# Performance work log

Hardware: AMD Instinct MI355X
Metric: run time of the kernel (lower is better)

The kernel has to match this reference:

```python
import jax, jax.numpy as jnp
import numpy as np

NUM_GRAPHS = 512


def setup_inputs() -> dict:
    key = jax.random.key(0)
    ks = jax.random.split(key, 16)
    N, E = 50000, 800000
    x = jax.random.normal(ks[0], (N, 3), dtype=jnp.float32)
    edge_index = jax.random.randint(ks[1], (2, E), 0, N, dtype=jnp.int64)
    batch = jnp.sort(jax.random.randint(ks[2], (N,), 0, NUM_GRAPHS, dtype=jnp.int64))

    def glorot(k, shape):
        fan_in, fan_out = shape
        lim = (6.0 / (fan_in + fan_out)) ** 0.5
        return jax.random.uniform(k, shape, jnp.float32, -lim, lim)

    return {
        "x": x, "edge_index": edge_index, "batch": batch,
        "W1": glorot(ks[3], (3, 32)),   "b1": jnp.zeros((32,), jnp.float32),
        "W2": glorot(ks[4], (32, 64)),  "b2": jnp.zeros((64,), jnp.float32),
        "W3": glorot(ks[5], (64, 128)), "b3": jnp.zeros((128,), jnp.float32),
        "Wf1": glorot(ks[6], (128, 32)), "bf1": jnp.zeros((32,), jnp.float32),
        "Wf2": glorot(ks[7], (32, 4)),   "bf2": jnp.zeros((4,), jnp.float32),
    }


def _gcn_conv(x, src, dst, norm, W, b, N):
    # GCNConv: h = x W, then symmetric-normalized aggregation, then bias.
    h = x @ W                                   # [N, out]
    msg = h[src] * norm[:, None]                # [E+N, out] gathered edge messages
    out = jax.ops.segment_sum(msg, dst, num_segments=N)
    return out + b


def reference(x, edge_index, batch, W1, b1, W2, b2, W3, b3, Wf1, bf1, Wf2, bf2):
    N = x.shape[0]
    loops = jnp.arange(N, dtype=edge_index.dtype)
    src = jnp.concatenate([edge_index[0], loops])   # add self-loops (GCNConv default)
    dst = jnp.concatenate([edge_index[1], loops])
    # symmetric normalization deg^-1/2[src] * deg^-1/2[dst], deg counted on dst
    deg = jax.ops.segment_sum(jnp.ones_like(dst, dtype=x.dtype), dst, num_segments=N)
    dinv = jnp.where(deg > 0, jax.lax.rsqrt(deg), 0.0)
    norm = dinv[src] * dinv[dst]                    # [E+N]

    h = jax.nn.relu(_gcn_conv(x, src, dst, norm, W1, b1, N))
    h = jax.nn.relu(_gcn_conv(h, src, dst, norm, W2, b2, N))
    h = jax.nn.relu(_gcn_conv(h, src, dst, norm, W3, b3, N))

    # global mean pool over graphs
    sums = jax.ops.segment_sum(h, batch, num_segments=NUM_GRAPHS)
    cnts = jax.ops.segment_sum(jnp.ones((N,), h.dtype), batch, num_segments=NUM_GRAPHS)
    pooled = sums / jnp.maximum(cnts, 1.0)[:, None]   # [G, 128]

    z = jax.nn.relu(pooled @ Wf1 + bf1)
    return z @ Wf2 + bf2                              # [G, 4]
```

## Files before the change

kernel.cpp:

```cpp
#include <hip/hip_runtime.h>

#define NN 50000
#define NE 800000
#define NG 512
#define CAP 64
#define NP 196
#define CH 3200
#define NCH 250

__global__ __launch_bounds__(256) void p1_hist_k(const int* __restrict__ dst,
                                                 int* __restrict__ Ht, int e) {
    __shared__ int lh[NP];
    int t = threadIdx.x, b = blockIdx.x;
    if (t < NP) lh[t] = 0;
    __syncthreads();
    int i0 = b * CH, i1 = min(e, i0 + CH);
    for (int i = i0 + t; i < i1; i += 256) atomicAdd(&lh[dst[i] >> 8], 1);
    __syncthreads();
    if (t < NP) Ht[t * NCH + b] = lh[t];
}

__global__ __launch_bounds__(256) void p2a_k(int* __restrict__ Ht, int* __restrict__ tot) {
    __shared__ int sh[256];
    int p = blockIdx.x, t = threadIdx.x;
    int v = (t < NCH) ? Ht[p * NCH + t] : 0;
    sh[t] = v;
    __syncthreads();
    for (int off = 1; off < 256; off <<= 1) {
        int x = (t >= off) ? sh[t - off] : 0;
        __syncthreads();
        sh[t] += x;
        __syncthreads();
    }
    if (t < NCH) Ht[p * NCH + t] = sh[t] - v;
    if (t == 255) tot[p] = sh[255];
}

__global__ __launch_bounds__(256) void p2b_k(const int* __restrict__ tot,
                                             int* __restrict__ start) {
    __shared__ int sh[256];
    int t = threadIdx.x;
    int v = (t < NP) ? tot[t] : 0;
    sh[t] = v;
    __syncthreads();
    for (int off = 1; off < 256; off <<= 1) {
        int x = (t >= off) ? sh[t - off] : 0;
        __syncthreads();
        sh[t] += x;
        __syncthreads();
    }
    if (t < NP) start[t] = sh[t] - v;
    if (t == 255) start[NP] = sh[255];
}

__global__ __launch_bounds__(256) void p3_place_k(const int* __restrict__ src,
                                                  const int* __restrict__ dst,
                                                  const int* __restrict__ Ht,
                                                  const int* __restrict__ start,
                                                  int* __restrict__ pak, int e) {
    __shared__ int cur[NP];
    int t = threadIdx.x, b = blockIdx.x;
    if (t < NP) cur[t] = start[t] + Ht[t * NCH + b];
    __syncthreads();
    int i0 = b * CH, i1 = min(e, i0 + CH);
    for (int i = i0 + t; i < i1; i += 256) {
        int d = dst[i], s = src[i];
        int p = d >> 8, dl = d & 255;
        int pos = atomicAdd(&cur[p], 1);
        pak[pos] = s | (dl << 16);
    }
}

__global__ __launch_bounds__(256) void p4_build_k(const int* __restrict__ pak,
                                                   const int* __restrict__ start,
                                                   const float* __restrict__ x,
                                                   int* __restrict__ fill,
                                                   float* __restrict__ dinv,
                                                   float* __restrict__ xs,
                                                   int* __restrict__ eidx, int n) {
    __shared__ int lh[256], curn[256];
    int p = blockIdx.x, t = threadIdx.x;
    lh[t] = 0;
    curn[t] = 0;
    __syncthreads();
    int s0 = start[p], s1 = start[p + 1];
    for (int i = s0 + t; i < s1; i += 256) atomicAdd(&lh[pak[i] >> 16], 1);
    __syncthreads();
    int node = p * 256 + t;
    if (node < n) {
        int dg = lh[t];
        fill[node] = dg;
        float d = rsqrtf((float)(dg + 1));
        dinv[node] = d;
        float4 v;
        v.x = x[node * 3 + 0] * d;
        v.y = x[node * 3 + 1] * d;
        v.z = x[node * 3 + 2] * d;
        v.w = 0.0f;
        *(float4*)(xs + (size_t)node * 4) = v;
    }
    __syncthreads();
    for (int i = s0 + t; i < s1; i += 256) {
        int w = pak[i];
        int dl = w >> 16, s = w & 0xFFFF;
        int pos = atomicAdd(&curn[dl], 1) & (CAP - 1);
        eidx[(size_t)(p * 256 + dl) * CAP + pos] = s;
    }
}

__global__ __launch_bounds__(256) void fused_l1_k(
    const int* __restrict__ deg, const int* __restrict__ eidx,
    const float* __restrict__ xs, const float* __restrict__ W1,
    const float* __restrict__ b1, const float* __restrict__ dinv,
    float* __restrict__ A2, int n) {
    __shared__ float act[64][4];
    int t = threadIdx.x;
    int node0 = blockIdx.x * 64;
    {
        int node = node0 + (t >> 2);
        int f = t & 3;
        if (node < n) {
            int e1 = deg[node];
            const int* __restrict__ eb = eidx + node * CAP;
            float acc = xs[(size_t)node * 4 + f];
            int e = 0;
            for (; e + 4 <= e1; e += 4) {
                int4 s = *(const int4*)(eb + e);
                float v0 = xs[(size_t)s.x * 4 + f];
                float v1 = xs[(size_t)s.y * 4 + f];
                float v2 = xs[(size_t)s.z * 4 + f];
                float v3 = xs[(size_t)s.w * 4 + f];
                acc += (v0 + v1) + (v2 + v3);
            }
            for (; e < e1; ++e) acc += xs[(size_t)eb[e] * 4 + f];
            act[t >> 2][f] = acc;
        }
    }
    __syncthreads();
    int f = t & 31;
    int nl0 = t >> 5;
#pragma unroll
    for (int i = 0; i < 8; ++i) {
        int nl = nl0 + i * 8;
        int node = node0 + nl;
        if (node < n) {
            float acc = act[nl][0] * W1[f] + act[nl][1] * W1[32 + f] + act[nl][2] * W1[64 + f];
            float s = dinv[node];
            A2[(size_t)node * 32 + f] = fmaxf(fmaf(s, acc, b1[f]), 0.0f) * s;
        }
    }
}

template <int F>
__global__ __launch_bounds__(256) void gather4_k(const int* __restrict__ deg,
                                                 const int* __restrict__ eidx,
                                                 const float* __restrict__ A,
                                                 float* __restrict__ B, int n) {
    constexpr int FV = F / 4;
    constexpr int NPB = 256 / FV;
    int t = threadIdx.x;
    int node = blockIdx.x * NPB + t / FV;
    int j = (t % FV) * 4;
    if (node >= n) return;
    int e1 = deg[node];
    const int* __restrict__ eb = eidx + node * CAP;
    const float* __restrict__ Aj = A + j;
    float4 a0 = *(const float4*)(Aj + (size_t)node * F);
    float4 a1 = make_float4(0.f, 0.f, 0.f, 0.f);
    float4 a2 = make_float4(0.f, 0.f, 0.f, 0.f);
    float4 a3 = make_float4(0.f, 0.f, 0.f, 0.f);
    int e = 0;
    for (; e + 16 <= e1; e += 16) {
        int4 sa = *(const int4*)(eb + e);
        int4 sb = *(const int4*)(eb + e + 4);
        int4 sc = *(const int4*)(eb + e + 8);
        int4 sd = *(const int4*)(eb + e + 12);
        float4 v0 = *(const float4*)(Aj + (size_t)sa.x * F);
        float4 v1 = *(const float4*)(Aj + (size_t)sa.y * F);
        float4 v2 = *(const float4*)(Aj + (size_t)sa.z * F);
        float4 v3 = *(const float4*)(Aj + (size_t)sa.w * F);
        float4 v4 = *(const float4*)(Aj + (size_t)sb.x * F);
        float4 v5 = *(const float4*)(Aj + (size_t)sb.y * F);
        float4 v6 = *(const float4*)(Aj + (size_t)sb.z * F);
        float4 v7 = *(const float4*)(Aj + (size_t)sb.w * F);
        float4 v8 = *(const float4*)(Aj + (size_t)sc.x * F);
        float4 v9 = *(const float4*)(Aj + (size_t)sc.y * F);
        float4 va = *(const float4*)(Aj + (size_t)sc.z * F);
        float4 vb = *(const float4*)(Aj + (size_t)sc.w * F);
        float4 vc = *(const float4*)(Aj + (size_t)sd.x * F);
        float4 vd = *(const float4*)(Aj + (size_t)sd.y * F);
        float4 ve = *(const float4*)(Aj + (size_t)sd.z * F);
        float4 vf = *(const float4*)(Aj + (size_t)sd.w * F);
        a0.x += (v0.x + v1.x) + (v2.x + v3.x);
        a0.y += (v0.y + v1.y) + (v2.y + v3.y);
        a0.z += (v0.z + v1.z) + (v2.z + v3.z);
        a0.w += (v0.w + v1.w) + (v2.w + v3.w);
        a1.x += (v4.x + v5.x) + (v6.x + v7.x);
        a1.y += (v4.y + v5.y) + (v6.y + v7.y);
        a1.z += (v4.z + v5.z) + (v6.z + v7.z);
        a1.w += (v4.w + v5.w) + (v6.w + v7.w);
        a2.x += (v8.x + v9.x) + (va.x + vb.x);
        a2.y += (v8.y + v9.y) + (va.y + vb.y);
        a2.z += (v8.z + v9.z) + (va.z + vb.z);
        a2.w += (v8.w + v9.w) + (va.w + vb.w);
        a3.x += (vc.x + vd.x) + (ve.x + vf.x);
        a3.y += (vc.y + vd.y) + (ve.y + vf.y);
        a3.z += (vc.z + vd.z) + (ve.z + vf.z);
        a3.w += (vc.w + vd.w) + (ve.w + vf.w);
    }
    for (; e + 4 <= e1; e += 4) {
        int4 sa = *(const int4*)(eb + e);
        float4 v0 = *(const float4*)(Aj + (size_t)sa.x * F);
        float4 v1 = *(const float4*)(Aj + (size_t)sa.y * F);
        float4 v2 = *(const float4*)(Aj + (size_t)sa.z * F);
        float4 v3 = *(const float4*)(Aj + (size_t)sa.w * F);
        a1.x += (v0.x + v1.x) + (v2.x + v3.x);
        a1.y += (v0.y + v1.y) + (v2.y + v3.y);
        a1.z += (v0.z + v1.z) + (v2.z + v3.z);
        a1.w += (v0.w + v1.w) + (v2.w + v3.w);
    }
    for (; e < e1; ++e) {
        float4 v = *(const float4*)(Aj + (size_t)eb[e] * F);
        a0.x += v.x; a0.y += v.y; a0.z += v.z; a0.w += v.w;
    }
    a0.x += (a1.x + a2.x) + a3.x;
    a0.y += (a1.y + a2.y) + a3.y;
    a0.z += (a1.z + a2.z) + a3.z;
    a0.w += (a1.w + a2.w) + a3.w;
    *(float4*)(B + (size_t)node * F + j) = a0;
}

template <int Fin, int Fout, int NPB, bool SCALE_OUT>
__global__ __launch_bounds__(256) void mmB_k(
    const float* __restrict__ G, const float* __restrict__ W,
    const float* __restrict__ bias, const float* __restrict__ dinv,
    float* __restrict__ Aout, int n) {
    constexpr int FL = Fout / 4;
    constexpr int NGRP = 256 / FL;
    constexpr int NPT = NPB / NGRP;
    __shared__ float act[NPB][Fin];
    int t = threadIdx.x;
    int node0 = blockIdx.x * NPB;
    constexpr int TOT4 = NPB * Fin / 4;
    const float4* __restrict__ G4 = (const float4*)(G + (size_t)node0 * Fin);
    float4* act4 = (float4*)&act[0][0];
    for (int i = t; i < TOT4; i += 256) {
        int nl = i / (Fin / 4);
        float4 v = make_float4(0.f, 0.f, 0.f, 0.f);
        if (node0 + nl < n) v = G4[i];
        act4[i] = v;
    }
    __syncthreads();
    int f4 = (t % FL) * 4;
    int nlbase = (t / FL) * NPT;
    float4 acc[NPT];
#pragma unroll
    for (int i = 0; i < NPT; ++i) acc[i] = make_float4(0.f, 0.f, 0.f, 0.f);
    for (int k = 0; k < Fin; k += 4) {
        float4 a[NPT];
#pragma unroll
        for (int i = 0; i < NPT; ++i) a[i] = *(const float4*)&act[nlbase + i][k];
#pragma unroll
        for (int kk = 0; kk < 4; ++kk) {
            float4 w = *(const float4*)(W + (size_t)(k + kk) * Fout + f4);
#pragma unroll
            for (int i = 0; i < NPT; ++i) {
                float av = (&a[i].x)[kk];
                acc[i].x = fmaf(av, w.x, acc[i].x);
                acc[i].y = fmaf(av, w.y, acc[i].y);
                acc[i].z = fmaf(av, w.z, acc[i].z);
                acc[i].w = fmaf(av, w.w, acc[i].w);
            }
        }
    }
    float4 bv = *(const float4*)(bias + f4);
#pragma unroll
    for (int i = 0; i < NPT; ++i) {
        int node = node0 + nlbase + i;
        if (node < n) {
            float s = dinv[node];
            float4 o;
            o.x = fmaxf(fmaf(s, acc[i].x, bv.x), 0.0f);
            o.y = fmaxf(fmaf(s, acc[i].y, bv.y), 0.0f);
            o.z = fmaxf(fmaf(s, acc[i].z, bv.z), 0.0f);
            o.w = fmaxf(fmaf(s, acc[i].w, bv.w), 0.0f);
            if (SCALE_OUT) { o.x *= s; o.y *= s; o.z *= s; o.w *= s; }
            *(float4*)(Aout + (size_t)node * Fout + f4) = o;
        }
    }
}

__device__ __forceinline__ int lbound_d(const int* __restrict__ a, int n, int key) {
    int lo = 0, hi = n;
    while (lo < hi) {
        int m = (lo + hi) >> 1;
        if (a[m] < key) lo = m + 1; else hi = m;
    }
    return lo;
}

__global__ __launch_bounds__(128) void poolhead_k(
    const float* __restrict__ H, const int* __restrict__ batch,
    const float* __restrict__ Wf1, const float* __restrict__ bf1,
    const float* __restrict__ Wf2, const float* __restrict__ bf2,
    float* __restrict__ out, int n) {
    __shared__ int bnd[2];
    __shared__ float pm[128];
    __shared__ float z[32];
    int g = blockIdx.x, t = threadIdx.x;
    if (t == 0) bnd[0] = lbound_d(batch, n, g);
    if (t == 1) bnd[1] = lbound_d(batch, n, g + 1);
    __syncthreads();
    int lo = bnd[0], hi = bnd[1];
    float s0 = 0.f, s1 = 0.f, s2 = 0.f, s3 = 0.f;
    int i = lo;
    for (; i + 4 <= hi; i += 4) {
        s0 += H[(size_t)i * 128 + t];
        s1 += H[(size_t)(i + 1) * 128 + t];
        s2 += H[(size_t)(i + 2) * 128 + t];
        s3 += H[(size_t)(i + 3) * 128 + t];
    }
    for (; i < hi; ++i) s0 += H[(size_t)i * 128 + t];
    float c = (float)(hi - lo);
    c = fmaxf(c, 1.0f);
    pm[t] = ((s0 + s1) + (s2 + s3)) / c;
    __syncthreads();
    if (t < 32) {
        float acc = bf1[t];
#pragma unroll 4
        for (int k = 0; k < 128; ++k) acc = fmaf(pm[k], Wf1[k * 32 + t], acc);
        z[t] = fmaxf(acc, 0.0f);
    }
    __syncthreads();
    if (t < 4) {
        float acc = bf2[t];
#pragma unroll
        for (int jj = 0; jj < 32; ++jj) acc = fmaf(z[jj], Wf2[jj * 4 + t], acc);
        out[g * 4 + t] = acc;
    }
}

extern "C" void kernel_launch(void* const* d_in, const int* in_sizes, int n_in,
                              void* d_out, int out_size, void* d_ws, size_t ws_size,
                              hipStream_t stream) {
    const float* x    = (const float*)d_in[0];
    const int*   ei   = (const int*)d_in[1];
    const int*   batch= (const int*)d_in[2];
    const float* W1   = (const float*)d_in[3];
    const float* b1   = (const float*)d_in[4];
    const float* W2   = (const float*)d_in[5];
    const float* b2   = (const float*)d_in[6];
    const float* W3   = (const float*)d_in[7];
    const float* b3   = (const float*)d_in[8];
    const float* Wf1  = (const float*)d_in[9];
    const float* bf1  = (const float*)d_in[10];
    const float* Wf2  = (const float*)d_in[11];
    const float* bf2  = (const float*)d_in[12];
    float* out = (float*)d_out;

    int*   fill   = (int*)d_ws;
    float* dinv   = (float*)(fill + NN);
    float* xs     = dinv + NN;
    float* A2     = xs + (size_t)NN * 4;
    float* A3     = A2 + (size_t)NN * 32;
    float* H3     = A3 + (size_t)NN * 64;
    float* G      = H3 + (size_t)NN * 128;
    int*   eidx   = (int*)(G + (size_t)NN * 64);

    int* pak   = (int*)G;
    int* Ht    = (int*)H3;
    int* tot   = Ht + NP * NCH;
    int* start = tot + 256;

    const int* src = ei;
    const int* dst = ei + NE;

    p1_hist_k<<<NCH, 256, 0, stream>>>(dst, Ht, NE);
    p2a_k<<<NP, 256, 0, stream>>>(Ht, tot);
    p2b_k<<<1, 256, 0, stream>>>(tot, start);
    p3_place_k<<<NCH, 256, 0, stream>>>(src, dst, Ht, start, pak, NE);
    p4_build_k<<<NP, 256, 0, stream>>>(pak, start, x, fill, dinv, xs, eidx, NN);

    fused_l1_k<<<(NN + 63) / 64, 256, 0, stream>>>(fill, eidx, xs, W1, b1, dinv, A2, NN);

    gather4_k<32><<<(NN + 31) / 32, 256, 0, stream>>>(fill, eidx, A2, G, NN);
    mmB_k<32, 64, 32, true><<<(NN + 31) / 32, 256, 0, stream>>>(G, W2, b2, dinv, A3, NN);

    gather4_k<64><<<(NN + 15) / 16, 256, 0, stream>>>(fill, eidx, A3, G, NN);
    mmB_k<64, 128, 32, false><<<(NN + 31) / 32, 256, 0, stream>>>(G, W3, b3, dinv, H3, NN);

    poolhead_k<<<NG, 128, 0, stream>>>(H3, batch, Wf1, bf1, Wf2, bf2, out, NN);
}
```

Before: 220.5 us.

## Switch to compact padded CSR and fuse gather with dense transform per layer

Replaces the fixed 64-slot-per-node edge table with a compact CSR. Each node's edge list is padded to a multiple of four and built in shared memory per 256-node partition, then copied out with vector stores. This cuts the edge-index footprint and the scattered writes. The separate gather and matmul kernels for layers 2 and 3 are fused into one kernel that aggregates into shared memory and then applies W, removing the intermediate G buffer round trip. The pooling kernel now uses 256 threads, splitting rows across two halves. Layer 3 now runs with 16 nodes per block, which lowers reuse of the weights, and the fixed SEG bound per partition risks overflow if a partition has too many edges.

Result: slower. 290.8 us (+31.9%).

```diff
diff --git a/kernel.cpp b/kernel.cpp
--- a/kernel.cpp
+++ b/kernel.cpp
@@ -3,10 +3,10 @@
 #define NN 50000
 #define NE 800000
 #define NG 512
-#define CAP 64
 #define NP 196
 #define CH 3200
 #define NCH 250
+#define SEG 6144
 
 __global__ __launch_bounds__(256) void p1_hist_k(const int* __restrict__ dst,
                                                  int* __restrict__ Ht, int e) {
@@ -72,24 +72,39 @@
 }
 
 __global__ __launch_bounds__(256) void p4_build_k(const int* __restrict__ pak,
-                                                   const int* __restrict__ start,
-                                                   const float* __restrict__ x,
-                                                   int* __restrict__ fill,
-                                                   float* __restrict__ dinv,
-                                                   float* __restrict__ xs,
-                                                   int* __restrict__ eidx, int n) {
-    __shared__ int lh[256], curn[256];
+                                                  const int* __restrict__ start,
+                                                  const float* __restrict__ x,
+                                                  int* __restrict__ fill,
+                                                  int* __restrict__ rowptr,
+                                                  float* __restrict__ dinv,
+                                                  float* __restrict__ xs,
+                                                  int* __restrict__ eidx, int n) {
+    __shared__ int lh[256], off[256], cnt[256], sh[256];
+    __shared__ int esort[SEG];
     int p = blockIdx.x, t = threadIdx.x;
     lh[t] = 0;
-    curn[t] = 0;
+    cnt[t] = 0;
     __syncthreads();
     int s0 = start[p], s1 = start[p + 1];
     for (int i = s0 + t; i < s1; i += 256) atomicAdd(&lh[pak[i] >> 16], 1);
     __syncthreads();
+    int dg = lh[t];
+    int padded = (dg + 3) & ~3;
+    sh[t] = padded;
+    __syncthreads();
+    for (int o = 1; o < 256; o <<= 1) {
+        int v = (t >= o) ? sh[t - o] : 0;
+        __syncthreads();
+        sh[t] += v;
+        __syncthreads();
+    }
+    int myoff = sh[t] - padded;
+    off[t] = myoff;
+    int total = sh[255];
     int node = p * 256 + t;
     if (node < n) {
-        int dg = lh[t];
         fill[node] = dg;
+        rowptr[node] = p * SEG + myoff;
         float d = rsqrtf((float)(dg + 1));
         dinv[node] = d;
         float4 v;
@@ -99,20 +114,26 @@
         v.w = 0.0f;
         *(float4*)(xs + (size_t)node * 4) = v;
     }
+    for (int i = t; i < total; i += 256) esort[i] = 0;
     __syncthreads();
     for (int i = s0 + t; i < s1; i += 256) {
         int w = pak[i];
         int dl = w >> 16, s = w & 0xFFFF;
-        int pos = atomicAdd(&curn[dl], 1) & (CAP - 1);
-        eidx[(size_t)(p * 256 + dl) * CAP + pos] = s;
-    }
+        int pos = atomicAdd(&cnt[dl], 1);
+        esort[off[dl] + pos] = s;
+    }
+    __syncthreads();
+    int4* eo = (int4*)(eidx + (size_t)p * SEG);
+    const int4* es = (const int4*)esort;
+    int tot4 = total >> 2;
+    for (int i = t; i < tot4; i += 256) eo[i] = es[i];
 }
 
 __global__ __launch_bounds__(256) void fused_l1_k(
-    const int* __restrict__ deg, const int* __restrict__ eidx,
-    const float* __restrict__ xs, const float* __restrict__ W1,
-    const float* __restrict__ b1, const float* __restrict__ dinv,
-    float* __restrict__ A2, int n) {
+    const int* __restrict__ deg, const int* __restrict__ rowptr,
+    const int* __restrict__ eidx, const float* __restrict__ xs,
+    const float* __restrict__ W1, const float* __restrict__ b1,
+    const float* __restrict__ dinv, float* __restrict__ A2, int n) {
     __shared__ float act[64][4];
     int t = threadIdx.x;
     int node0 = blockIdx.x * 64;
@@ -121,7 +142,7 @@
         int f = t & 3;
         if (node < n) {
             int e1 = deg[node];
-            const int* __restrict__ eb = eidx + node * CAP;
+            const int* __restrict__ eb = eidx + rowptr[node];
             float acc = xs[(size_t)node * 4 + f];
             int e = 0;
             for (; e + 4 <= e1; e += 4) {
@@ -151,106 +172,94 @@
     }
 }
 
-template <int F>
-__global__ __launch_bounds__(256) void gather4_k(const int* __restrict__ deg,
-                                                 const int* __restrict__ eidx,
-                                                 const float* __restrict__ A,
-                                                 float* __restrict__ B, int n) {
-    constexpr int FV = F / 4;
-    constexpr int NPB = 256 / FV;
+template <int Fin, int Fout, int NPB, bool SCALE_OUT>
+__global__ __launch_bounds__(256) void fused_gmm_k(
+    const int* __restrict__ deg, const int* __restrict__ rowptr,
+    const int* __restrict__ eidx, const float* __restrict__ A,
+    const float* __restrict__ W, const float* __restrict__ bias,
+    const float* __restrict__ dinv, float* __restrict__ Aout, int n) {
+    constexpr int FV = Fin / 4;
+    static_assert(NPB * FV == 256, "block geometry");
+    __shared__ float act[NPB][Fin];
     int t = threadIdx.x;
-    int node = blockIdx.x * NPB + t / FV;
-    int j = (t % FV) * 4;
-    if (node >= n) return;
-    int e1 = deg[node];
-    const int* __restrict__ eb = eidx + node * CAP;
-    const float* __restrict__ Aj = A + j;
-    float4 a0 = *(const float4*)(Aj + (size_t)node * F);
-    float4 a1 = make_float4(0.f, 0.f, 0.f, 0.f);
-    float4 a2 = make_float4(0.f, 0.f, 0.f, 0.f);
-    float4 a3 = make_float4(0.f, 0.f, 0.f, 0.f);
-    int e = 0;
-    for (; e + 16 <= e1; e += 16) {
-        int4 sa = *(const int4*)(eb + e);
-        int4 sb = *(const int4*)(eb + e + 4);
-        int4 sc = *(const int4*)(eb + e + 8);
-        int4 sd = *(const int4*)(eb + e + 12);
-        float4 v0 = *(const float4*)(Aj + (size_t)sa.x * F);
-        float4 v1 = *(const float4*)(Aj + (size_t)sa.y * F);
-        float4 v2 = *(const float4*)(Aj + (size_t)sa.z * F);
-        float4 v3 = *(const float4*)(Aj + (size_t)sa.w * F);
-        float4 v4 = *(const float4*)(Aj + (size_t)sb.x * F);
-        float4 v5 = *(const float4*)(Aj + (size_t)sb.y * F);
-        float4 v6 = *(const float4*)(Aj + (size_t)sb.z * F);
-        float4 v7 = *(const float4*)(Aj + (size_t)sb.w * F);
-        float4 v8 = *(const float4*)(Aj + (size_t)sc.x * F);
-        float4 v9 = *(const float4*)(Aj + (size_t)sc.y * F);
-        float4 va = *(const float4*)(Aj + (size_t)sc.z * F);
-        float4 vb = *(const float4*)(Aj + (size_t)sc.w * F);
-        float4 vc = *(const float4*)(Aj + (size_t)sd.x * F);
-        float4 vd = *(const float4*)(Aj + (size_t)sd.y * F);
-        float4 ve = *(const float4*)(Aj + (size_t)sd.z * F);
-        float4 vf = *(const float4*)(Aj + (size_t)sd.w * F);
-        a0.x += (v0.x + v1.x) + (v2.x + v3.x);
-        a0.y += (v0.y + v1.y) + (v2.y + v3.y);
-        a0.z += (v0.z + v1.z) + (v2.z + v3.z);
-        a0.w += (v0.w + v1.w) + (v2.w + v3.w);
-        a1.x += (v4.x + v5.x) + (v6.x + v7.x);
-        a1.y += (v4.y + v5.y) + (v6.y + v7.y);
-        a1.z += (v4.z + v5.z) + (v6.z + v7.z);
-        a1.w += (v4.w + v5.w) + (v6.w + v7.w);
-        a2.x += (v8.x + v9.x) + (va.x + vb.x);
-        a2.y += (v8.y + v9.y) + (va.y + vb.y);
-        a2.z += (v8.z + v9.z) + (va.z + vb.z);
-        a2.w += (v8.w + v9.w) + (va.w + vb.w);
-        a3.x += (vc.x + vd.x) + (ve.x + vf.x);
-        a3.y += (vc.y + vd.y) + (ve.y + vf.y);
-        a3.z += (vc.z + vd.z) + (ve.z + vf.z);
-        a3.w += (vc.w + vd.w) + (ve.w + vf.w);
-    }
-    for (; e + 4 <= e1; e += 4) {
-        int4 sa = *(const int4*)(eb + e);
-        float4 v0 = *(const float4*)(Aj + (size_t)sa.x * F);
-        float4 v1 = *(const float4*)(Aj + (size_t)sa.y * F);
-        float4 v2 = *(const float4*)(Aj + (size_t)sa.z * F);
-        float4 v3 = *(const float4*)(Aj + (size_t)sa.w * F);
-        a1.x += (v0.x + v1.x) + (v2.x + v3.x);
-        a1.y += (v0.y + v1.y) + (v2.y + v3.y);
-        a1.z += (v0.z + v1.z) + (v2.z + v3.z);
-        a1.w += (v0.w + v1.w) + (v2.w + v3.w);
-    }
-    for (; e < e1; ++e) {
-        float4 v = *(const float4*)(Aj + (size_t)eb[e] * F);
-        a0.x += v.x; a0.y += v.y; a0.z += v.z; a0.w += v.w;
-    }
-    a0.x += (a1.x + a2.x) + a3.x;
-    a0.y += (a1.y + a2.y) + a3.y;
-    a0.z += (a1.z + a2.z) + a3.z;
-    a0.w += (a1.w + a2.w) + a3.w;
-    *(float4*)(B + (size_t)node * F + j) = a0;
-}
-
-template <int Fin, int Fout, int NPB, bool SCALE_OUT>
-__global__ __launch_bounds__(256) void mmB_k(
-    const float* __restrict__ G, const float* __restrict__ W,
-    const float* __restrict__ bias, const float* __restrict__ dinv,
-    float* __restrict__ Aout, int n) {
+    int node0 = blockIdx.x * NPB;
+    {
+        int node = node0 + t / FV;
+        int j = (t % FV) * 4;
+        float4 a0 = make_float4(0.f, 0.f, 0.f, 0.f);
+        if (node < n) {
+            const float* __restrict__ Aj = A + j;
+            int e1 = deg[node];
+            const int* __restrict__ eb = eidx + rowptr[node];
+            a0 = *(const float4*)(Aj + (size_t)node * Fin);
+            float4 a1 = make_float4(0.f, 0.f, 0.f, 0.f);
+            float4 a2 = make_float4(0.f, 0.f, 0.f, 0.f);
+            float4 a3 = make_float4(0.f, 0.f, 0.f, 0.f);
+            int e = 0;
+            for (; e + 16 <= e1; e += 16) {
+                int4 sa = *(const int4*)(eb + e);
+                int4 sb = *(const int4*)(eb + e + 4);
+                int4 sc = *(const int4*)(eb + e + 8);
+                int4 sd = *(const int4*)(eb + e + 12);
+                float4 v0 = *(const float4*)(Aj + (size_t)sa.x * Fin);
+                float4 v1 = *(const float4*)(Aj + (size_t)sa.y * Fin);
+                float4 v2 = *(const float4*)(Aj + (size_t)sa.z * Fin);
+                float4 v3 = *(const float4*)(Aj + (size_t)sa.w * Fin);
+                float4 v4 = *(const float4*)(Aj + (size_t)sb.x * Fin);
+                float4 v5 = *(const float4*)(Aj + (size_t)sb.y * Fin);
+                float4 v6 = *(const float4*)(Aj + (size_t)sb.z * Fin);
+                float4 v7 = *(const float4*)(Aj + (size_t)sb.w * Fin);
+                float4 v8 = *(const float4*)(Aj + (size_t)sc.x * Fin);
+                float4 v9 = *(const float4*)(Aj + (size_t)sc.y * Fin);
+                float4 va = *(const float4*)(Aj + (size_t)sc.z * Fin);
+                float4 vb = *(const float4*)(Aj + (size_t)sc.w * Fin);
+                float4 vc = *(const float4*)(Aj + (size_t)sd.x * Fin);
+                float4 vd = *(const float4*)(Aj + (size_t)sd.y * Fin);
+                float4 ve = *(const float4*)(Aj + (size_t)sd.z * Fin);
+                float4 vf = *(const float4*)(Aj + (size_t)sd.w * Fin);
+                a0.x += (v0.x + v1.x) + (v2.x + v3.x);
+                a0.y += (v0.y + v1.y) + (v2.y + v3.y);
+                a0.z += (v0.z + v1.z) + (v2.z + v3.z);
+                a0.w += (v0.w + v1.w) + (v2.w + v3.w);
+                a1.x += (v4.x + v5.x) + (v6.x + v7.x);
+                a1.y += (v4.y + v5.y) + (v6.y + v7.y);
+                a1.z += (v4.z + v5.z) + (v6.z + v7.z);
+                a1.w += (v4.w + v5.w) + (v6.w + v7.w);
+                a2.x += (v8.x + v9.x) + (va.x + vb.x);
+                a2.y += (v8.y + v9.y) + (va.y + vb.y);
+                a2.z += (v8.z + v9.z) + (va.z + vb.z);
+                a2.w += (v8.w + v9.w) + (va.w + vb.w);
+                a3.x += (vc.x + vd.x) + (ve.x + vf.x);
+                a3.y += (vc.y + vd.y) + (ve.y + vf.y);
+                a3.z += (vc.z + vd.z) + (ve.z + vf.z);
+                a3.w += (vc.w + vd.w) + (ve.w + vf.w);
+            }
+            for (; e + 4 <= e1; e += 4) {
+                int4 sa = *(const int4*)(eb + e);
+                float4 v0 = *(const float4*)(Aj + (size_t)sa.x * Fin);
+                float4 v1 = *(const float4*)(Aj + (size_t)sa.y * Fin);
+                float4 v2 = *(const float4*)(Aj + (size_t)sa.z * Fin);
+                float4 v3 = *(const float4*)(Aj + (size_t)sa.w * Fin);
+                a1.x += (v0.x + v1.x) + (v2.x + v3.x);
+                a1.y += (v0.y + v1.y) + (v2.y + v3.y);
+                a1.z += (v0.z + v1.z) + (v2.z + v3.z);
+                a1.w += (v0.w + v1.w) + (v2.w + v3.w);
+            }
+            for (; e < e1; ++e) {
+                float4 v = *(const float4*)(Aj + (size_t)eb[e] * Fin);
+                a0.x += v.x; a0.y += v.y; a0.z += v.z; a0.w += v.w;
+            }
+            a0.x += (a1.x + a2.x) + a3.x;
+            a0.y += (a1.y + a2.y) + a3.y;
+            a0.z += (a1.z + a2.z) + a3.z;
+            a0.w += (a1.w + a2.w) + a3.w;
+        }
+        *(float4*)&act[t / FV][j] = a0;
+    }
+    __syncthreads();
     constexpr int FL = Fout / 4;
     constexpr int NGRP = 256 / FL;
     constexpr int NPT = NPB / NGRP;
-    __shared__ float act[NPB][Fin];
-    int t = threadIdx.x;
-    int node0 = blockIdx.x * NPB;
-    constexpr int TOT4 = NPB * Fin / 4;
-    const float4* __restrict__ G4 = (const float4*)(G + (size_t)node0 * Fin);
-    float4* act4 = (float4*)&act[0][0];
-    for (int i = t; i < TOT4; i += 256) {
-        int nl = i / (Fin / 4);
-        float4 v = make_float4(0.f, 0.f, 0.f, 0.f);
-        if (node0 + nl < n) v = G4[i];
-        act4[i] = v;
-    }
-    __syncthreads();
     int f4 = (t % FL) * 4;
     int nlbase = (t / FL) * NPT;
     float4 acc[NPT];
@@ -299,31 +308,35 @@
     return lo;
 }
 
-__global__ __launch_bounds__(128) void poolhead_k(
+__global__ __launch_bounds__(256) void poolhead_k(
     const float* __restrict__ H, const int* __restrict__ batch,
     const float* __restrict__ Wf1, const float* __restrict__ bf1,
     const float* __restrict__ Wf2, const float* __restrict__ bf2,
     float* __restrict__ out, int n) {
     __shared__ int bnd[2];
+    __shared__ float part[256];
     __shared__ float pm[128];
     __shared__ float z[32];
     int g = blockIdx.x, t = threadIdx.x;
-    if (t == 0) bnd[0] = lbound_d(batch, n, g);
-    if (t == 1) bnd[1] = lbound_d(batch, n, g + 1);
+    if (t < 2) bnd[t] = lbound_d(batch, n, g + t);
     __syncthreads();
     int lo = bnd[0], hi = bnd[1];
+    int c = t & 127, h = t >> 7;
     float s0 = 0.f, s1 = 0.f, s2 = 0.f, s3 = 0.f;
-    int i = lo;
-    for (; i + 4 <= hi; i += 4) {
-        s0 += H[(size_t)i * 128 + t];
-        s1 += H[(size_t)(i + 1) * 128 + t];
-        s2 += H[(size_t)(i + 2) * 128 + t];
-        s3 += H[(size_t)(i + 3) * 128 + t];
-    }
-    for (; i < hi; ++i) s0 += H[(size_t)i * 128 + t];
-    float c = (float)(hi - lo);
-    c = fmaxf(c, 1.0f);
-    pm[t] = ((s0 + s1) + (s2 + s3)) / c;
+    int i = lo + h;
+    for (; i + 6 < hi; i += 8) {
+        s0 += H[(size_t)i * 128 + c];
+        s1 += H[(size_t)(i + 2) * 128 + c];
+        s2 += H[(size_t)(i + 4) * 128 + c];
+        s3 += H[(size_t)(i + 6) * 128 + c];
+    }
+    for (; i < hi; i += 2) s0 += H[(size_t)i * 128 + c];
+    part[t] = (s0 + s1) + (s2 + s3);
+    __syncthreads();
+    if (t < 128) {
+        float cn = fmaxf((float)(hi - lo), 1.0f);
+        pm[t] = (part[t] + part[t + 128]) / cn;
+    }
     __syncthreads();
     if (t < 32) {
         float acc = bf1[t];
@@ -360,15 +373,15 @@
 
     int*   fill   = (int*)d_ws;
     float* dinv   = (float*)(fill + NN);
-    float* xs     = dinv + NN;
+    int*   rowptr = (int*)(dinv + NN);
+    float* xs     = (float*)(rowptr + NN);
     float* A2     = xs + (size_t)NN * 4;
     float* A3     = A2 + (size_t)NN * 32;
     float* H3     = A3 + (size_t)NN * 64;
-    float* G      = H3 + (size_t)NN * 128;
-    int*   eidx   = (int*)(G + (size_t)NN * 64);
-
-    int* pak   = (int*)G;
-    int* Ht    = (int*)H3;
+    int*   eidx   = (int*)(H3 + (size_t)NN * 128);
+
+    int* pak   = (int*)H3;
+    int* Ht    = (int*)A3;
     int* tot   = Ht + NP * NCH;
     int* start = tot + 256;
 
@@ -379,15 +392,15 @@
     p2a_k<<<NP, 256, 0, stream>>>(Ht, tot);
     p2b_k<<<1, 256, 0, stream>>>(tot, start);
     p3_place_k<<<NCH, 256, 0, stream>>>(src, dst, Ht, start, pak, NE);
-    p4_build_k<<<NP, 256, 0, stream>>>(pak, start, x, fill, dinv, xs, eidx, NN);
-
-    fused_l1_k<<<(NN + 63) / 64, 256, 0, stream>>>(fill, eidx, xs, W1, b1, dinv, A2, NN);
-
-    gather4_k<32><<<(NN + 31) / 32, 256, 0, stream>>>(fill, eidx, A2, G, NN);
-    mmB_k<32, 64, 32, true><<<(NN + 31) / 32, 256, 0, stream>>>(G, W2, b2, dinv, A3, NN);
-
-    gather4_k<64><<<(NN + 15) / 16, 256, 0, stream>>>(fill, eidx, A3, G, NN);
-    mmB_k<64, 128, 32, false><<<(NN + 31) / 32, 256, 0, stream>>>(G, W3, b3, dinv, H3, NN);
-
-    poolhead_k<<<NG, 128, 0, stream>>>(H3, batch, Wf1, bf1, Wf2, bf2, out, NN);
-}
+    p4_build_k<<<NP, 256, 0, stream>>>(pak, start, x, fill, rowptr, dinv, xs, eidx, NN);
+
+    fused_l1_k<<<(NN + 63) / 64, 256, 0, stream>>>(fill, rowptr, eidx, xs, W1, b1, dinv, A2, NN);
+
+    fused_gmm_k<32, 64, 32, true><<<(NN + 31) / 32, 256, 0, stream>>>(
+        fill, rowptr, eidx, A2, W2, b2, dinv, A3, NN);
+
+    fused_gmm_k<64, 128, 16, false><<<(NN + 15) / 16, 256, 0, stream>>>(
+        fill, rowptr, eidx, A3, W3, b3, dinv, H3, NN);
+
+    poolhead_k<<<NG, 256, 0, stream>>>(H3, batch, Wf1, bf1, Wf2, bf2, out, NN);
+}
```

## Replace fixed-capacity edge slots with compact padded CSR built in shared memory

Applied to the files above, without the earlier changes.

Edge lists per destination node are now packed contiguously per 256-node partition, with 4-aligned padded offsets computed by a shared-memory scan and a rowptr array, instead of fixed 64-entry slots. This shrinks the index footprint and improves cache-line utilization in the gather kernels, and removes the silent wraparound for high-degree nodes. It also adds an occupancy hint to the gather kernel and splits the pooling reduction across 256 threads. It risks overflowing the per-partition segment if a partition exceeds SEG edges.

Measured after the change: 229.6 us. 1.04x slower.

```diff
diff --git a/kernel.cpp b/kernel.cpp
--- a/kernel.cpp
+++ b/kernel.cpp
@@ -3,10 +3,10 @@
 #define NN 50000
 #define NE 800000
 #define NG 512
-#define CAP 64
 #define NP 196
 #define CH 3200
 #define NCH 250
+#define SEG 6144
 
 __global__ __launch_bounds__(256) void p1_hist_k(const int* __restrict__ dst,
                                                  int* __restrict__ Ht, int e) {
@@ -72,24 +72,39 @@
 }
 
 __global__ __launch_bounds__(256) void p4_build_k(const int* __restrict__ pak,
-                                                   const int* __restrict__ start,
-                                                   const float* __restrict__ x,
-                                                   int* __restrict__ fill,
-                                                   float* __restrict__ dinv,
-                                                   float* __restrict__ xs,
-                                                   int* __restrict__ eidx, int n) {
-    __shared__ int lh[256], curn[256];
+                                                  const int* __restrict__ start,
+                                                  const float* __restrict__ x,
+                                                  int* __restrict__ fill,
+                                                  int* __restrict__ rowptr,
+                                                  float* __restrict__ dinv,
+                                                  float* __restrict__ xs,
+                                                  int* __restrict__ eidx, int n) {
+    __shared__ int lh[256], off[256], cnt[256], sh[256];
+    __shared__ int esort[SEG];
     int p = blockIdx.x, t = threadIdx.x;
     lh[t] = 0;
-    curn[t] = 0;
+    cnt[t] = 0;
     __syncthreads();
     int s0 = start[p], s1 = start[p + 1];
     for (int i = s0 + t; i < s1; i += 256) atomicAdd(&lh[pak[i] >> 16], 1);
     __syncthreads();
+    int dg = lh[t];
+    int padded = (dg + 3) & ~3;
+    sh[t] = padded;
+    __syncthreads();
+    for (int o = 1; o < 256; o <<= 1) {
+        int v = (t >= o) ? sh[t - o] : 0;
+        __syncthreads();
+        sh[t] += v;
+        __syncthreads();
+    }
+    int myoff = sh[t] - padded;
+    off[t] = myoff;
+    int total = sh[255];
     int node = p * 256 + t;
     if (node < n) {
-        int dg = lh[t];
         fill[node] = dg;
+        rowptr[node] = p * SEG + myoff;
         float d = rsqrtf((float)(dg + 1));
         dinv[node] = d;
         float4 v;
@@ -99,20 +114,26 @@
         v.w = 0.0f;
         *(float4*)(xs + (size_t)node * 4) = v;
     }
+    for (int i = t; i < total; i += 256) esort[i] = 0;
     __syncthreads();
     for (int i = s0 + t; i < s1; i += 256) {
         int w = pak[i];
         int dl = w >> 16, s = w & 0xFFFF;
-        int pos = atomicAdd(&curn[dl], 1) & (CAP - 1);
-        eidx[(size_t)(p * 256 + dl) * CAP + pos] = s;
-    }
+        int pos = atomicAdd(&cnt[dl], 1);
+        esort[off[dl] + pos] = s;
+    }
+    __syncthreads();
+    int4* eo = (int4*)(eidx + (size_t)p * SEG);
+    const int4* es = (const int4*)esort;
+    int tot4 = total >> 2;
+    for (int i = t; i < tot4; i += 256) eo[i] = es[i];
 }
 
 __global__ __launch_bounds__(256) void fused_l1_k(
-    const int* __restrict__ deg, const int* __restrict__ eidx,
-    const float* __restrict__ xs, const float* __restrict__ W1,
-    const float* __restrict__ b1, const float* __restrict__ dinv,
-    float* __restrict__ A2, int n) {
+    const int* __restrict__ deg, const int* __restrict__ rowptr,
+    const int* __restrict__ eidx, const float* __restrict__ xs,
+    const float* __restrict__ W1, const float* __restrict__ b1,
+    const float* __restrict__ dinv, float* __restrict__ A2, int n) {
     __shared__ float act[64][4];
     int t = threadIdx.x;
     int node0 = blockIdx.x * 64;
@@ -121,7 +142,7 @@
         int f = t & 3;
         if (node < n) {
             int e1 = deg[node];
-            const int* __restrict__ eb = eidx + node * CAP;
+            const int* __restrict__ eb = eidx + rowptr[node];
             float acc = xs[(size_t)node * 4 + f];
             int e = 0;
             for (; e + 4 <= e1; e += 4) {
@@ -152,10 +173,11 @@
 }
 
 template <int F>
-__global__ __launch_bounds__(256) void gather4_k(const int* __restrict__ deg,
-                                                 const int* __restrict__ eidx,
-                                                 const float* __restrict__ A,
-                                                 float* __restrict__ B, int n) {
+__global__ __launch_bounds__(256, 4) void gather4_k(const int* __restrict__ deg,
+                                                    const int* __restrict__ rowptr,
+                                                    const int* __restrict__ eidx,
+                                                    const float* __restrict__ A,
+                                                    float* __restrict__ B, int n) {
     constexpr int FV = F / 4;
     constexpr int NPB = 256 / FV;
     int t = threadIdx.x;
@@ -163,7 +185,7 @@
     int j = (t % FV) * 4;
     if (node >= n) return;
     int e1 = deg[node];
-    const int* __restrict__ eb = eidx + node * CAP;
+    const int* __restrict__ eb = eidx + rowptr[node];
     const float* __restrict__ Aj = A + j;
     float4 a0 = *(const float4*)(Aj + (size_t)node * F);
     float4 a1 = make_float4(0.f, 0.f, 0.f, 0.f);
@@ -299,31 +321,35 @@
     return lo;
 }
 
-__global__ __launch_bounds__(128) void poolhead_k(
+__global__ __launch_bounds__(256) void poolhead_k(
     const float* __restrict__ H, const int* __restrict__ batch,
     const float* __restrict__ Wf1, const float* __restrict__ bf1,
     const float* __restrict__ Wf2, const float* __restrict__ bf2,
     float* __restrict__ out, int n) {
     __shared__ int bnd[2];
+    __shared__ float part[256];
     __shared__ float pm[128];
     __shared__ float z[32];
     int g = blockIdx.x, t = threadIdx.x;
-    if (t == 0) bnd[0] = lbound_d(batch, n, g);
-    if (t == 1) bnd[1] = lbound_d(batch, n, g + 1);
+    if (t < 2) bnd[t] = lbound_d(batch, n, g + t);
     __syncthreads();
     int lo = bnd[0], hi = bnd[1];
+    int c = t & 127, h = t >> 7;
     float s0 = 0.f, s1 = 0.f, s2 = 0.f, s3 = 0.f;
-    int i = lo;
-    for (; i + 4 <= hi; i += 4) {
-        s0 += H[(size_t)i * 128 + t];
-        s1 += H[(size_t)(i + 1) * 128 + t];
-        s2 += H[(size_t)(i + 2) * 128 + t];
-        s3 += H[(size_t)(i + 3) * 128 + t];
-    }
-    for (; i < hi; ++i) s0 += H[(size_t)i * 128 + t];
-    float c = (float)(hi - lo);
-    c = fmaxf(c, 1.0f);
-    pm[t] = ((s0 + s1) + (s2 + s3)) / c;
+    int i = lo + h;
+    for (; i + 6 < hi; i += 8) {
+        s0 += H[(size_t)i * 128 + c];
+        s1 += H[(size_t)(i + 2) * 128 + c];
+        s2 += H[(size_t)(i + 4) * 128 + c];
+        s3 += H[(size_t)(i + 6) * 128 + c];
+    }
+    for (; i < hi; i += 2) s0 += H[(size_t)i * 128 + c];
+    part[t] = (s0 + s1) + (s2 + s3);
+    __syncthreads();
+    if (t < 128) {
+        float cn = fmaxf((float)(hi - lo), 1.0f);
+        pm[t] = (part[t] + part[t + 128]) / cn;
+    }
     __syncthreads();
     if (t < 32) {
         float acc = bf1[t];
@@ -360,7 +386,8 @@
 
     int*   fill   = (int*)d_ws;
     float* dinv   = (float*)(fill + NN);
-    float* xs     = dinv + NN;
+    int*   rowptr = (int*)(dinv + NN);
+    float* xs     = (float*)(rowptr + NN);
     float* A2     = xs + (size_t)NN * 4;
     float* A3     = A2 + (size_t)NN * 32;
     float* H3     = A3 + (size_t)NN * 64;
@@ -379,15 +406,15 @@
     p2a_k<<<NP, 256, 0, stream>>>(Ht, tot);
     p2b_k<<<1, 256, 0, stream>>>(tot, start);
     p3_place_k<<<NCH, 256, 0, stream>>>(src, dst, Ht, start, pak, NE);
-    p4_build_k<<<NP, 256, 0, stream>>>(pak, start, x, fill, dinv, xs, eidx, NN);
-
-    fused_l1_k<<<(NN + 63) / 64, 256, 0, stream>>>(fill, eidx, xs, W1, b1, dinv, A2, NN);
-
-    gather4_k<32><<<(NN + 31) / 32, 256, 0, stream>>>(fill, eidx, A2, G, NN);
+    p4_build_k<<<NP, 256, 0, stream>>>(pak, start, x, fill, rowptr, dinv, xs, eidx, NN);
+
+    fused_l1_k<<<(NN + 63) / 64, 256, 0, stream>>>(fill, rowptr, eidx, xs, W1, b1, dinv, A2, NN);
+
+    gather4_k<32><<<(NN + 31) / 32, 256, 0, stream>>>(fill, rowptr, eidx, A2, G, NN);
     mmB_k<32, 64, 32, true><<<(NN + 31) / 32, 256, 0, stream>>>(G, W2, b2, dinv, A3, NN);
 
-    gather4_k<64><<<(NN + 15) / 16, 256, 0, stream>>>(fill, eidx, A3, G, NN);
+    gather4_k<64><<<(NN + 15) / 16, 256, 0, stream>>>(fill, rowptr, eidx, A3, G, NN);
     mmB_k<64, 128, 32, false><<<(NN + 31) / 32, 256, 0, stream>>>(G, W3, b3, dinv, H3, NN);
 
-    poolhead_k<<<NG, 128, 0, stream>>>(H3, batch, Wf1, bf1, Wf2, bf2, out, NN);
-}
+    poolhead_k<<<NG, 256, 0, stream>>>(H3, batch, Wf1, bf1, Wf2, bf2, out, NN);
+}
```
